# Kernel optimization log

Measured on AMD Instinct MI355X. Metric: run time of the kernel, lower is better.

## Reference

```python
import jax, jax.numpy as jnp
import numpy as np
import math

EMBED_DIM = 1024
NUM_HEADS = 16
HEAD_DIM = EMBED_DIM // NUM_HEADS
BATCH = 2
SEQ = 2048


def alibi_slopes(num_heads):
    def pow2_slopes(n):
        start = 2.0 ** (-(2.0 ** (-(math.log2(n) - 3))))
        return [start * (start ** i) for i in range(n)]
    if math.log2(num_heads).is_integer():
        s = pow2_slopes(num_heads)
    else:
        closest = 2 ** math.floor(math.log2(num_heads))
        s = pow2_slopes(closest)
        s += s[-1:] * (num_heads - closest)
    return jnp.asarray(s, dtype=jnp.float32)  # [H]


def setup_inputs() -> dict:
    key = jax.random.key(0)
    k1, k2, k3, k4, k5 = jax.random.split(key, 5)
    x = jax.random.normal(k1, (BATCH, SEQ, EMBED_DIM), dtype=jnp.float32)
    sd = 1.0 / math.sqrt(EMBED_DIM)
    Wqkv = jax.random.uniform(k2, (EMBED_DIM, 3 * EMBED_DIM), minval=-sd, maxval=sd, dtype=jnp.float32)
    bqkv = jax.random.uniform(k3, (3 * EMBED_DIM,), minval=-sd, maxval=sd, dtype=jnp.float32)
    Wout = jax.random.uniform(k4, (EMBED_DIM, EMBED_DIM), minval=-sd, maxval=sd, dtype=jnp.float32)
    bout = jax.random.uniform(k5, (EMBED_DIM,), minval=-sd, maxval=sd, dtype=jnp.float32)
    return {"x": x, "Wqkv": Wqkv, "bqkv": bqkv, "Wout": Wout, "bout": bout}


def reference(x, Wqkv, bqkv, Wout, bout):
    B, S, E = x.shape
    H, D = NUM_HEADS, HEAD_DIM
    qkv = x @ Wqkv + bqkv                       # [B,S,3E]
    qkv = qkv.reshape(B, S, H, 3 * D)
    q, k, v = jnp.split(qkv, 3, axis=-1)        # each [B,S,H,D]
    scores = jnp.einsum('bqhd,bkhd->bhqk', q, k) / math.sqrt(D)
    # ALiBi bias: distance[i,j] = j - i, scaled per-head
    pos = jnp.arange(S)
    distance = (pos[None, :] - pos[:, None]).astype(jnp.float32)  # [S,S]
    scores = scores + alibi_slopes(H)[None, :, None, None] * distance[None, None, :, :]
    attn = jax.nn.softmax(scores, axis=-1)      # [B,H,S,S]
    out = jnp.einsum('bhqk,bkhd->bqhd', attn, v).reshape(B, S, E)
    out = out @ Wout + bout
    return out, attn
```

## Files before the change

kernel.cpp:

```cpp
#include <hip/hip_runtime.h>

#define BATCH 2
#define SEQ   2048
#define EMB   1024
#define NH    16
#define HD    64

typedef __attribute__((ext_vector_type(8))) _Float16 half8;
typedef __attribute__((ext_vector_type(4))) _Float16 half4;
typedef __attribute__((ext_vector_type(4))) float floatx4;

#define LOG2E 1.44269504088896f

#if __has_builtin(__builtin_amdgcn_exp2f)
__device__ __forceinline__ float fexp2(float x) { return __builtin_amdgcn_exp2f(x); }
#else
__device__ __forceinline__ float fexp2(float x) { return exp2f(x); }
#endif

__global__ __launch_bounds__(256)
void cvt_f16(const float* __restrict__ in, _Float16* __restrict__ out, int n8) {
    int i = blockIdx.x * 256 + threadIdx.x;
    if (i >= n8) return;
    float4 a = ((const float4*)in)[2 * i];
    float4 b = ((const float4*)in)[2 * i + 1];
    half8 h = {(_Float16)a.x, (_Float16)a.y, (_Float16)a.z, (_Float16)a.w,
               (_Float16)b.x, (_Float16)b.y, (_Float16)b.z, (_Float16)b.w};
    ((half8*)out)[i] = h;
}

__global__ __launch_bounds__(256)
void transpose_f16(const float* __restrict__ W, _Float16* __restrict__ o,
                   int K, int N) {
    __shared__ float t[32][33];
    const int n0 = blockIdx.x * 32, k0 = blockIdx.y * 32;
    const int r = threadIdx.x >> 3, c4 = (threadIdx.x & 7) * 4;
    float4 v = *(const float4*)&W[(size_t)(k0 + r) * N + n0 + c4];
    t[r][c4 + 0] = v.x; t[r][c4 + 1] = v.y;
    t[r][c4 + 2] = v.z; t[r][c4 + 3] = v.w;
    __syncthreads();
    half4 hv;
#pragma unroll
    for (int j = 0; j < 4; ++j) hv[j] = (_Float16)t[c4 + j][r];
    *(half4*)&o[(size_t)(n0 + r) * K + k0 + c4] = hv;
}

#define ALD 40

__global__ __launch_bounds__(256)
void gemm_qkv_mfma(const _Float16* __restrict__ Xh, const _Float16* __restrict__ Wh,
                   const float* __restrict__ bias,
                   _Float16* __restrict__ Qh, _Float16* __restrict__ Kh,
                   _Float16* __restrict__ Vh) {
    const int K = EMB;
    __shared__ _Float16 Ah[2][128 * ALD];
    __shared__ _Float16 Bh[2][128 * ALD];

    const int tid  = threadIdx.x;
    const int wave = tid >> 6, lane = tid & 63;
    const int quad = lane >> 4, lp = lane & 15;

    const int linear = blockIdx.y * 24 + blockIdx.x;
    const int swz = (linear & 7) * 96 + (linear >> 3);
    const int bx = swz % 24, by = swz / 24;
    const int row0 = by * 128, col0 = bx * 128;
    const int wm = (wave >> 1) * 64, wn = (wave & 1) * 64;

    const int srow = tid >> 2, sseg = (tid & 3) * 8;

    floatx4 acc[4][4];
#pragma unroll
    for (int i = 0; i < 4; ++i)
#pragma unroll
        for (int j = 0; j < 4; ++j) acc[i][j] = (floatx4){0.f, 0.f, 0.f, 0.f};

    uint4 a0 = *(const uint4*)&Xh[(size_t)(row0 + srow) * K + sseg];
    uint4 a1 = *(const uint4*)&Xh[(size_t)(row0 + srow + 64) * K + sseg];
    uint4 b0 = *(const uint4*)&Wh[(size_t)(col0 + srow) * K + sseg];
    uint4 b1 = *(const uint4*)&Wh[(size_t)(col0 + srow + 64) * K + sseg];
    *(uint4*)&Ah[0][srow * ALD + sseg] = a0;
    *(uint4*)&Ah[0][(srow + 64) * ALD + sseg] = a1;
    *(uint4*)&Bh[0][srow * ALD + sseg] = b0;
    *(uint4*)&Bh[0][(srow + 64) * ALD + sseg] = b1;

    int cur = 0;
    for (int k0 = 0; k0 < K; k0 += 32) {
        __syncthreads();
        if (k0 + 32 < K) {
            a0 = *(const uint4*)&Xh[(size_t)(row0 + srow) * K + k0 + 32 + sseg];
            a1 = *(const uint4*)&Xh[(size_t)(row0 + srow + 64) * K + k0 + 32 + sseg];
            b0 = *(const uint4*)&Wh[(size_t)(col0 + srow) * K + k0 + 32 + sseg];
            b1 = *(const uint4*)&Wh[(size_t)(col0 + srow + 64) * K + k0 + 32 + sseg];
        }

        half8 ah[4];
#pragma unroll
        for (int mi = 0; mi < 4; ++mi)
            ah[mi] = *(const half8*)&Ah[cur][(wm + mi * 16 + lp) * ALD + quad * 8];
#pragma unroll
        for (int ni = 0; ni < 4; ++ni) {
            half8 bh = *(const half8*)&Bh[cur][(wn + ni * 16 + lp) * ALD + quad * 8];
#pragma unroll
            for (int mi = 0; mi < 4; ++mi)
                acc[mi][ni] = __builtin_amdgcn_mfma_f32_16x16x32_f16(
                    ah[mi], bh, acc[mi][ni], 0, 0, 0);
        }

        if (k0 + 32 < K) {
            *(uint4*)&Ah[cur ^ 1][srow * ALD + sseg] = a0;
            *(uint4*)&Ah[cur ^ 1][(srow + 64) * ALD + sseg] = a1;
            *(uint4*)&Bh[cur ^ 1][srow * ALD + sseg] = b0;
            *(uint4*)&Bh[cur ^ 1][(srow + 64) * ALD + sseg] = b1;
            cur ^= 1;
        }
    }

#pragma unroll
    for (int ni = 0; ni < 4; ++ni) {
        const int c = col0 + wn + ni * 16 + lp;
        const int h = c / 192;
        const int rem = c - h * 192;
        const int which = rem >> 6;
        const int d = rem & 63;
        _Float16* __restrict__ P = (which == 0) ? Qh : (which == 1) ? Kh : Vh;
        const float bb = bias[c];
#pragma unroll
        for (int mi = 0; mi < 4; ++mi) {
            floatx4 a = acc[mi][ni];
#pragma unroll
            for (int r = 0; r < 4; ++r) {
                int m = row0 + wm + mi * 16 + quad * 4 + r;
                int b = m >> 11, s = m & (SEQ - 1);
                P[((size_t)(b * NH + h) * SEQ + s) * HD + d] =
                    (_Float16)(a[r] + bb);
            }
        }
    }
}

__global__ __launch_bounds__(256)
void gemm_out_mfma(const _Float16* __restrict__ Ch, const _Float16* __restrict__ Oh,
                   const float* __restrict__ bias, float* __restrict__ out) {
    const int K = EMB, N = EMB;
    __shared__ _Float16 Ah[2][128 * ALD];
    __shared__ _Float16 Bh[2][128 * ALD];

    const int tid  = threadIdx.x;
    const int wave = tid >> 6, lane = tid & 63;
    const int quad = lane >> 4, lp = lane & 15;

    const int linear = blockIdx.y * 8 + blockIdx.x;
    const int swz = (linear & 7) * 32 + (linear >> 3);
    const int bx = swz & 7, by = swz >> 3;
    const int row0 = by * 128, col0 = bx * 128;
    const int wm = (wave >> 1) * 64, wn = (wave & 1) * 64;

    const int srow = tid >> 2, sseg = (tid & 3) * 8;

    floatx4 acc[4][4];
#pragma unroll
    for (int i = 0; i < 4; ++i)
#pragma unroll
        for (int j = 0; j < 4; ++j) acc[i][j] = (floatx4){0.f, 0.f, 0.f, 0.f};

    uint4 a0 = *(const uint4*)&Ch[(size_t)(row0 + srow) * K + sseg];
    uint4 a1 = *(const uint4*)&Ch[(size_t)(row0 + srow + 64) * K + sseg];
    uint4 b0 = *(const uint4*)&Oh[(size_t)(col0 + srow) * K + sseg];
    uint4 b1 = *(const uint4*)&Oh[(size_t)(col0 + srow + 64) * K + sseg];
    *(uint4*)&Ah[0][srow * ALD + sseg] = a0;
    *(uint4*)&Ah[0][(srow + 64) * ALD + sseg] = a1;
    *(uint4*)&Bh[0][srow * ALD + sseg] = b0;
    *(uint4*)&Bh[0][(srow + 64) * ALD + sseg] = b1;

    int cur = 0;
    for (int k0 = 0; k0 < K; k0 += 32) {
        __syncthreads();
        if (k0 + 32 < K) {
            a0 = *(const uint4*)&Ch[(size_t)(row0 + srow) * K + k0 + 32 + sseg];
            a1 = *(const uint4*)&Ch[(size_t)(row0 + srow + 64) * K + k0 + 32 + sseg];
            b0 = *(const uint4*)&Oh[(size_t)(col0 + srow) * K + k0 + 32 + sseg];
            b1 = *(const uint4*)&Oh[(size_t)(col0 + srow + 64) * K + k0 + 32 + sseg];
        }

        half8 ah[4];
#pragma unroll
        for (int mi = 0; mi < 4; ++mi)
            ah[mi] = *(const half8*)&Ah[cur][(wm + mi * 16 + lp) * ALD + quad * 8];
#pragma unroll
        for (int ni = 0; ni < 4; ++ni) {
            half8 bh = *(const half8*)&Bh[cur][(wn + ni * 16 + lp) * ALD + quad * 8];
#pragma unroll
            for (int mi = 0; mi < 4; ++mi)
                acc[mi][ni] = __builtin_amdgcn_mfma_f32_16x16x32_f16(
                    ah[mi], bh, acc[mi][ni], 0, 0, 0);
        }

        if (k0 + 32 < K) {
            *(uint4*)&Ah[cur ^ 1][srow * ALD + sseg] = a0;
            *(uint4*)&Ah[cur ^ 1][(srow + 64) * ALD + sseg] = a1;
            *(uint4*)&Bh[cur ^ 1][srow * ALD + sseg] = b0;
            *(uint4*)&Bh[cur ^ 1][(srow + 64) * ALD + sseg] = b1;
            cur ^= 1;
        }
    }

#pragma unroll
    for (int ni = 0; ni < 4; ++ni) {
        const int c = col0 + wn + ni * 16 + lp;
        const float bb = bias[c];
#pragma unroll
        for (int mi = 0; mi < 4; ++mi) {
            floatx4 a = acc[mi][ni];
#pragma unroll
            for (int r = 0; r < 4; ++r) {
                int m = row0 + wm + mi * 16 + quad * 4 + r;
                out[(size_t)m * N + c] = a[r] + bb;
            }
        }
    }
}

#define QT 128
#define KT 64
#define LDST 72
#define NTILE (SEQ / KT)

__global__ __launch_bounds__(512)
void attn_mfma(const _Float16* __restrict__ Qh,
               const _Float16* __restrict__ Kh,
               const _Float16* __restrict__ Vh,
               float* __restrict__ attn,
               _Float16* __restrict__ ctx) {
    __shared__ _Float16 ksb[2][KT * LDST];
    __shared__ _Float16 vtb[2][HD * LDST];
    __shared__ _Float16 ps[QT * LDST];

    const int tid  = threadIdx.x;
    const int wave = tid >> 6, lane = tid & 63;
    const int quad = lane >> 4, lp = lane & 15;
    const int q0 = blockIdx.x * QT;
    const int bh = blockIdx.y;
    const int h  = bh & (NH - 1);
    const float slope2 = exp2f(-0.5f * (float)(h + 1)) * LOG2E;
    const float scale2 = 0.125f * LOG2E;

    const _Float16* Qbase = Qh + ((size_t)bh * SEQ + q0) * HD;
    const _Float16* Kbase = Kh + (size_t)bh * SEQ * HD;
    const _Float16* Vbase = Vh + (size_t)bh * SEQ * HD;

    const half8 qa0 = *(const half8*)&Qbase[(size_t)(16 * wave + lp) * HD + quad * 8];
    const half8 qa1 = *(const half8*)&Qbase[(size_t)(16 * wave + lp) * HD + 32 + quad * 8];

    const int qg = q0 + 16 * wave + lp;
    const float aq = -slope2 * (float)qg;

    const int srow = tid >> 3, sseg = tid & 7;
    const int kvx = srow ^ (sseg << 3);

    float m0 = -1e30f, mxv = -1e30f, lsum = 0.f;

    uint4 kreg = *(const uint4*)&Kbase[(size_t)srow * HD + sseg * 8];
    *(uint4*)&ksb[0][srow * LDST + sseg * 8] = kreg;
    __syncthreads();

    int cur = 0;
    for (int kt = 0; kt < NTILE; ++kt) {
        if (kt) __syncthreads();
        if (kt + 1 < NTILE)
            kreg = *(const uint4*)&Kbase[(size_t)(kt + 1) * KT * HD +
                                         (size_t)srow * HD + sseg * 8];
        const _Float16* ks = ksb[cur];

        floatx4 cc[4];
        __builtin_amdgcn_s_setprio(1);
#pragma unroll
        for (int t = 0; t < 4; ++t) {
            half8 b0 = *(const half8*)&ks[(16 * t + lp) * LDST + quad * 8];
            half8 b1 = *(const half8*)&ks[(16 * t + lp) * LDST + 32 + quad * 8];
            floatx4 c = {0.f, 0.f, 0.f, 0.f};
            c = __builtin_amdgcn_mfma_f32_16x16x32_f16(b0, qa0, c, 0, 0, 0);
            cc[t] = __builtin_amdgcn_mfma_f32_16x16x32_f16(b1, qa1, c, 0, 0, 0);
        }
        __builtin_amdgcn_s_setprio(0);
#pragma unroll
        for (int t = 0; t < 4; ++t) {
            float kb = (float)(kt * KT + 16 * t + 4 * quad);
            float s0 = fmaf(cc[t][0], scale2, fmaf(slope2, kb,       aq));
            float s1 = fmaf(cc[t][1], scale2, fmaf(slope2, kb + 1.f, aq));
            float s2 = fmaf(cc[t][2], scale2, fmaf(slope2, kb + 2.f, aq));
            float s3 = fmaf(cc[t][3], scale2, fmaf(slope2, kb + 3.f, aq));
            float tm = fmaxf(fmaxf(s0, s1), fmaxf(s2, s3));
            mxv = fmaxf(mxv, tm);
            if (mxv > m0 + 8.f) {
                lsum *= fexp2(m0 - mxv);
                m0 = mxv;
            }
            lsum += fexp2(s0 - m0) + fexp2(s1 - m0) +
                    fexp2(s2 - m0) + fexp2(s3 - m0);
        }

        if (kt + 1 < NTILE) {
            *(uint4*)&ksb[cur ^ 1][srow * LDST + sseg * 8] = kreg;
            cur ^= 1;
        }
    }

    float off2;
    {
        float mm = mxv;
        float ll = lsum * fexp2(m0 - mm);
#pragma unroll
        for (int off = 16; off < 64; off <<= 1) {
            float mo = __shfl_xor(mm, off);
            float lo = __shfl_xor(ll, off);
            float mn = fmaxf(mm, mo);
            ll = ll * fexp2(mm - mn) + lo * fexp2(mo - mn);
            mm = mn;
        }
        off2 = mm + __log2f(ll);
    }

    floatx4 o[4];
#pragma unroll
    for (int t = 0; t < 4; ++t) o[t] = (floatx4){0.f, 0.f, 0.f, 0.f};

    float* arow = attn + (size_t)bh * SEQ * SEQ +
                  (size_t)(q0 + 16 * wave + lp) * SEQ + 4 * quad;
    const float aq2 = aq - off2;

    __syncthreads();
    uint4 vreg;
    kreg = *(const uint4*)&Kbase[(size_t)srow * HD + sseg * 8];
    vreg = *(const uint4*)&Vbase[(size_t)srow * HD + sseg * 8];
    *(uint4*)&ksb[0][srow * LDST + sseg * 8] = kreg;
    {
        union { uint4 u; _Float16 e[8]; } vv; vv.u = vreg;
#pragma unroll
        for (int j = 0; j < 8; ++j)
            vtb[0][(sseg * 8 + j) * LDST + kvx] = vv.e[j];
    }
    __syncthreads();

    cur = 0;
    for (int kt = 0; kt < NTILE; ++kt) {
        if (kt) __syncthreads();
        if (kt + 1 < NTILE) {
            size_t goff = (size_t)(kt + 1) * KT * HD + (size_t)srow * HD + sseg * 8;
            kreg = *(const uint4*)&Kbase[goff];
            vreg = *(const uint4*)&Vbase[goff];
        }
        const _Float16* ks = ksb[cur];
        const _Float16* vt = vtb[cur];

        __builtin_amdgcn_s_setprio(1);
#pragma unroll
        for (int t = 0; t < 4; ++t) {
            half8 b0 = *(const half8*)&ks[(16 * t + lp) * LDST + quad * 8];
            half8 b1 = *(const half8*)&ks[(16 * t + lp) * LDST + 32 + quad * 8];
            floatx4 c = {0.f, 0.f, 0.f, 0.f};
            c = __builtin_amdgcn_mfma_f32_16x16x32_f16(b0, qa0, c, 0, 0, 0);
            c = __builtin_amdgcn_mfma_f32_16x16x32_f16(b1, qa1, c, 0, 0, 0);
            float kb = (float)(kt * KT + 16 * t + 4 * quad);
            float p0 = fexp2(fmaf(c[0], scale2, fmaf(slope2, kb,       aq2)));
            float p1 = fexp2(fmaf(c[1], scale2, fmaf(slope2, kb + 1.f, aq2)));
            float p2 = fexp2(fmaf(c[2], scale2, fmaf(slope2, kb + 2.f, aq2)));
            float p3 = fexp2(fmaf(c[3], scale2, fmaf(slope2, kb + 3.f, aq2)));
            float4 pw = {p0, p1, p2, p3};
            *(float4*)&arow[kt * KT + 16 * t] = pw;
            const int col = 16 * t + 4 * quad;
            half4 ph = {(_Float16)p0, (_Float16)p1, (_Float16)p2, (_Float16)p3};
            *(half4*)&ps[(16 * wave + lp) * LDST + col] = ph;
        }
        __builtin_amdgcn_s_setprio(0);

        half8 pa0 = *(const half8*)&ps[(16 * wave + lp) * LDST + quad * 8];
        half8 pa1 = *(const half8*)&ps[(16 * wave + lp) * LDST + 32 + quad * 8];
        __builtin_amdgcn_s_setprio(1);
#pragma unroll
        for (int t = 0; t < 4; ++t) {
            int g = 2 * t + (lp >> 3);
            half8 vb0 = *(const half8*)&vt[(16 * t + lp) * LDST + ((quad ^ g) << 3)];
            half8 vb1 = *(const half8*)&vt[(16 * t + lp) * LDST + (((quad + 4) ^ g) << 3)];
            o[t] = __builtin_amdgcn_mfma_f32_16x16x32_f16(pa0, vb0, o[t], 0, 0, 0);
            o[t] = __builtin_amdgcn_mfma_f32_16x16x32_f16(pa1, vb1, o[t], 0, 0, 0);
        }
        __builtin_amdgcn_s_setprio(0);

        if (kt + 1 < NTILE) {
            *(uint4*)&ksb[cur ^ 1][srow * LDST + sseg * 8] = kreg;
            union { uint4 u; _Float16 e[8]; } vv; vv.u = vreg;
#pragma unroll
            for (int j = 0; j < 8; ++j)
                vtb[cur ^ 1][(sseg * 8 + j) * LDST + kvx] = vv.e[j];
            cur ^= 1;
        }
    }

    const int b = bh >> 4;
#pragma unroll
    for (int t = 0; t < 4; ++t)
#pragma unroll
        for (int r = 0; r < 4; ++r)
            ctx[((size_t)(b * SEQ + q0 + 16 * wave + quad * 4 + r)) * EMB +
                h * HD + 16 * t + lp] = (_Float16)o[t][r];
}


extern "C" void kernel_launch(void* const* d_in, const int* in_sizes, int n_in,
                              void* d_out, int out_size, void* d_ws, size_t ws_size,
                              hipStream_t stream) {
    const float* x    = (const float*)d_in[0];
    const float* Wqkv = (const float*)d_in[1];
    const float* bqkv = (const float*)d_in[2];
    const float* Wout = (const float*)d_in[3];
    const float* bout = (const float*)d_in[4];

    float* out  = (float*)d_out;
    float* attn = out + (size_t)BATCH * SEQ * EMB;

    const size_t HE = (size_t)BATCH * NH * SEQ * HD;
    const size_t XE = (size_t)BATCH * SEQ * EMB;
    _Float16* Qh = (_Float16*)d_ws;
    _Float16* Kh = Qh + HE;
    _Float16* Vh = Kh + HE;
    _Float16* Ch = Vh + HE;
    _Float16* Xh = Ch + XE;
    _Float16* Wh = Xh + XE;
    _Float16* Oh = Wh + (size_t)3 * EMB * EMB;

    cvt_f16<<<dim3(2048), dim3(256), 0, stream>>>(x, Xh, (int)(XE / 8));
    transpose_f16<<<dim3(96, 32), dim3(256), 0, stream>>>(Wqkv, Wh, EMB, 3 * EMB);
    transpose_f16<<<dim3(32, 32), dim3(256), 0, stream>>>(Wout, Oh, EMB, EMB);

    gemm_qkv_mfma<<<dim3(24, 32), dim3(256), 0, stream>>>(
        Xh, Wh, bqkv, Qh, Kh, Vh);

    attn_mfma<<<dim3(SEQ / QT, BATCH * NH), dim3(512), 0, stream>>>(
        Qh, Kh, Vh, attn, Ch);

    gemm_out_mfma<<<dim3(8, 32), dim3(256), 0, stream>>>(Ch, Oh, bout, out);
}
```

Measured before the change: 258.8 us.

## Load GEMM tiles directly to LDS and relax attention barriers

Both the QKV and output-projection GEMMs now use global_load_lds to move their double-buffered tiles straight from global memory into LDS, with no register staging. The LDS row stride drops from 40 to 32 halves so that each lane's 16-byte destination is contiguous with the lane index, which the direct load requires. The attention kernel replaces __syncthreads with a barrier that waits only on lgkmcnt, so in-flight global prefetches into registers are not drained at every tile. The trade-off is that the unpadded GEMM tiles may cause LDS bank conflicts on the fragment reads.

```diff
diff --git a/kernel.cpp b/kernel.cpp
--- a/kernel.cpp
+++ b/kernel.cpp
@@ -17,6 +17,19 @@
 #else
 __device__ __forceinline__ float fexp2(float x) { return exp2f(x); }
 #endif
+
+__device__ __forceinline__ void gl2lds16(const _Float16* gp, _Float16* lp_) {
+    __builtin_amdgcn_global_load_lds(
+        (const __attribute__((address_space(1))) unsigned int*)gp,
+        (__attribute__((address_space(3))) unsigned int*)lp_,
+        16, 0, 0);
+}
+
+__device__ __forceinline__ void lds_barrier() {
+    asm volatile("s_waitcnt lgkmcnt(0)" ::: "memory");
+    __builtin_amdgcn_s_barrier();
+    __builtin_amdgcn_sched_barrier(0);
+}
 
 __global__ __launch_bounds__(256)
 void cvt_f16(const float* __restrict__ in, _Float16* __restrict__ out, int n8) {
@@ -45,7 +58,7 @@
     *(half4*)&o[(size_t)(n0 + r) * K + k0 + c4] = hv;
 }
 
-#define ALD 40
+#define ALD 32
 
 __global__ __launch_bounds__(256)
 void gemm_qkv_mfma(const _Float16* __restrict__ Xh, const _Float16* __restrict__ Wh,
@@ -74,23 +87,24 @@
 #pragma unroll
         for (int j = 0; j < 4; ++j) acc[i][j] = (floatx4){0.f, 0.f, 0.f, 0.f};
 
-    uint4 a0 = *(const uint4*)&Xh[(size_t)(row0 + srow) * K + sseg];
-    uint4 a1 = *(const uint4*)&Xh[(size_t)(row0 + srow + 64) * K + sseg];
-    uint4 b0 = *(const uint4*)&Wh[(size_t)(col0 + srow) * K + sseg];
-    uint4 b1 = *(const uint4*)&Wh[(size_t)(col0 + srow + 64) * K + sseg];
-    *(uint4*)&Ah[0][srow * ALD + sseg] = a0;
-    *(uint4*)&Ah[0][(srow + 64) * ALD + sseg] = a1;
-    *(uint4*)&Bh[0][srow * ALD + sseg] = b0;
-    *(uint4*)&Bh[0][(srow + 64) * ALD + sseg] = b1;
+    gl2lds16(&Xh[(size_t)(row0 + srow) * K + sseg],      &Ah[0][srow * ALD + sseg]);
+    gl2lds16(&Xh[(size_t)(row0 + srow + 64) * K + sseg], &Ah[0][(srow + 64) * ALD + sseg]);
+    gl2lds16(&Wh[(size_t)(col0 + srow) * K + sseg],      &Bh[0][srow * ALD + sseg]);
+    gl2lds16(&Wh[(size_t)(col0 + srow + 64) * K + sseg], &Bh[0][(srow + 64) * ALD + sseg]);
 
     int cur = 0;
     for (int k0 = 0; k0 < K; k0 += 32) {
         __syncthreads();
         if (k0 + 32 < K) {
-            a0 = *(const uint4*)&Xh[(size_t)(row0 + srow) * K + k0 + 32 + sseg];
-            a1 = *(const uint4*)&Xh[(size_t)(row0 + srow + 64) * K + k0 + 32 + sseg];
-            b0 = *(const uint4*)&Wh[(size_t)(col0 + srow) * K + k0 + 32 + sseg];
-            b1 = *(const uint4*)&Wh[(size_t)(col0 + srow + 64) * K + k0 + 32 + sseg];
+            int kn = k0 + 32;
+            gl2lds16(&Xh[(size_t)(row0 + srow) * K + kn + sseg],
+                     &Ah[cur ^ 1][srow * ALD + sseg]);
+            gl2lds16(&Xh[(size_t)(row0 + srow + 64) * K + kn + sseg],
+                     &Ah[cur ^ 1][(srow + 64) * ALD + sseg]);
+            gl2lds16(&Wh[(size_t)(col0 + srow) * K + kn + sseg],
+                     &Bh[cur ^ 1][srow * ALD + sseg]);
+            gl2lds16(&Wh[(size_t)(col0 + srow + 64) * K + kn + sseg],
+                     &Bh[cur ^ 1][(srow + 64) * ALD + sseg]);
         }
 
         half8 ah[4];
@@ -106,13 +120,7 @@
                     ah[mi], bh, acc[mi][ni], 0, 0, 0);
         }
 
-        if (k0 + 32 < K) {
-            *(uint4*)&Ah[cur ^ 1][srow * ALD + sseg] = a0;
-            *(uint4*)&Ah[cur ^ 1][(srow + 64) * ALD + sseg] = a1;
-            *(uint4*)&Bh[cur ^ 1][srow * ALD + sseg] = b0;
-            *(uint4*)&Bh[cur ^ 1][(srow + 64) * ALD + sseg] = b1;
-            cur ^= 1;
-        }
+        if (k0 + 32 < K) cur ^= 1;
     }
 
 #pragma unroll
@@ -163,23 +171,24 @@
 #pragma unroll
         for (int j = 0; j < 4; ++j) acc[i][j] = (floatx4){0.f, 0.f, 0.f, 0.f};
 
-    uint4 a0 = *(const uint4*)&Ch[(size_t)(row0 + srow) * K + sseg];
-    uint4 a1 = *(const uint4*)&Ch[(size_t)(row0 + srow + 64) * K + sseg];
-    uint4 b0 = *(const uint4*)&Oh[(size_t)(col0 + srow) * K + sseg];
-    uint4 b1 = *(const uint4*)&Oh[(size_t)(col0 + srow + 64) * K + sseg];
-    *(uint4*)&Ah[0][srow * ALD + sseg] = a0;
-    *(uint4*)&Ah[0][(srow + 64) * ALD + sseg] = a1;
-    *(uint4*)&Bh[0][srow * ALD + sseg] = b0;
-    *(uint4*)&Bh[0][(srow + 64) * ALD + sseg] = b1;
+    gl2lds16(&Ch[(size_t)(row0 + srow) * K + sseg],      &Ah[0][srow * ALD + sseg]);
+    gl2lds16(&Ch[(size_t)(row0 + srow + 64) * K + sseg], &Ah[0][(srow + 64) * ALD + sseg]);
+    gl2lds16(&Oh[(size_t)(col0 + srow) * K + sseg],      &Bh[0][srow * ALD + sseg]);
+    gl2lds16(&Oh[(size_t)(col0 + srow + 64) * K + sseg], &Bh[0][(srow + 64) * ALD + sseg]);
 
     int cur = 0;
     for (int k0 = 0; k0 < K; k0 += 32) {
         __syncthreads();
         if (k0 + 32 < K) {
-            a0 = *(const uint4*)&Ch[(size_t)(row0 + srow) * K + k0 + 32 + sseg];
-            a1 = *(const uint4*)&Ch[(size_t)(row0 + srow + 64) * K + k0 + 32 + sseg];
-            b0 = *(const uint4*)&Oh[(size_t)(col0 + srow) * K + k0 + 32 + sseg];
-            b1 = *(const uint4*)&Oh[(size_t)(col0 + srow + 64) * K + k0 + 32 + sseg];
+            int kn = k0 + 32;
+            gl2lds16(&Ch[(size_t)(row0 + srow) * K + kn + sseg],
+                     &Ah[cur ^ 1][srow * ALD + sseg]);
+            gl2lds16(&Ch[(size_t)(row0 + srow + 64) * K + kn + sseg],
+                     &Ah[cur ^ 1][(srow + 64) * ALD + sseg]);
+            gl2lds16(&Oh[(size_t)(col0 + srow) * K + kn + sseg],
+                     &Bh[cur ^ 1][srow * ALD + sseg]);
+            gl2lds16(&Oh[(size_t)(col0 + srow + 64) * K + kn + sseg],
+                     &Bh[cur ^ 1][(srow + 64) * ALD + sseg]);
         }
 
         half8 ah[4];
@@ -195,13 +204,7 @@
                     ah[mi], bh, acc[mi][ni], 0, 0, 0);
         }
 
-        if (k0 + 32 < K) {
-            *(uint4*)&Ah[cur ^ 1][srow * ALD + sseg] = a0;
-            *(uint4*)&Ah[cur ^ 1][(srow + 64) * ALD + sseg] = a1;
-            *(uint4*)&Bh[cur ^ 1][srow * ALD + sseg] = b0;
-            *(uint4*)&Bh[cur ^ 1][(srow + 64) * ALD + sseg] = b1;
-            cur ^= 1;
-        }
+        if (k0 + 32 < K) cur ^= 1;
     }
 
 #pragma unroll
@@ -261,11 +264,11 @@
 
     uint4 kreg = *(const uint4*)&Kbase[(size_t)srow * HD + sseg * 8];
     *(uint4*)&ksb[0][srow * LDST + sseg * 8] = kreg;
-    __syncthreads();
+    lds_barrier();
 
     int cur = 0;
     for (int kt = 0; kt < NTILE; ++kt) {
-        if (kt) __syncthreads();
+        if (kt) lds_barrier();
         if (kt + 1 < NTILE)
             kreg = *(const uint4*)&Kbase[(size_t)(kt + 1) * KT * HD +
                                          (size_t)srow * HD + sseg * 8];
@@ -328,7 +331,7 @@
                   (size_t)(q0 + 16 * wave + lp) * SEQ + 4 * quad;
     const float aq2 = aq - off2;
 
-    __syncthreads();
+    lds_barrier();
     uint4 vreg;
     kreg = *(const uint4*)&Kbase[(size_t)srow * HD + sseg * 8];
     vreg = *(const uint4*)&Vbase[(size_t)srow * HD + sseg * 8];
@@ -339,11 +342,11 @@
         for (int j = 0; j < 8; ++j)
             vtb[0][(sseg * 8 + j) * LDST + kvx] = vv.e[j];
     }
-    __syncthreads();
+    lds_barrier();
 
     cur = 0;
     for (int kt = 0; kt < NTILE; ++kt) {
-        if (kt) __syncthreads();
+        if (kt) lds_barrier();
         if (kt + 1 < NTILE) {
             size_t goff = (size_t)(kt + 1) * KT * HD + (size_t)srow * HD + sseg * 8;
             kreg = *(const uint4*)&Kbase[goff];
```

New measurement: 263.5 us. No clear change (+1.8%).

## Fuse x fp16 conversion into QKV GEMM, merge weight transposes, lighten barriers

Applied to the files above, without the earlier changes.

Removes the standalone x-to-fp16 conversion kernel: the QKV GEMM now loads fp32 x tiles directly and converts them to half before writing to LDS. The two weight transpose launches are combined into one kernel with a larger grid. The attention kernel's __syncthreads calls are replaced by a custom barrier that waits only on LDS counters, so outstanding global prefetches are not forced to drain. The aim is fewer launches and less intermediate traffic, at the cost of the GEMM reading twice as many bytes for x on each re-read.

```diff
diff --git a/kernel.cpp b/kernel.cpp
--- a/kernel.cpp
+++ b/kernel.cpp
@@ -18,22 +18,21 @@
 __device__ __forceinline__ float fexp2(float x) { return exp2f(x); }
 #endif
 
+__device__ __forceinline__ void lds_barrier() {
+    asm volatile("s_waitcnt lgkmcnt(0)" ::: "memory");
+    __builtin_amdgcn_s_barrier();
+    __builtin_amdgcn_sched_barrier(0);
+}
+
 __global__ __launch_bounds__(256)
-void cvt_f16(const float* __restrict__ in, _Float16* __restrict__ out, int n8) {
-    int i = blockIdx.x * 256 + threadIdx.x;
-    if (i >= n8) return;
-    float4 a = ((const float4*)in)[2 * i];
-    float4 b = ((const float4*)in)[2 * i + 1];
-    half8 h = {(_Float16)a.x, (_Float16)a.y, (_Float16)a.z, (_Float16)a.w,
-               (_Float16)b.x, (_Float16)b.y, (_Float16)b.z, (_Float16)b.w};
-    ((half8*)out)[i] = h;
-}
-
-__global__ __launch_bounds__(256)
-void transpose_f16(const float* __restrict__ W, _Float16* __restrict__ o,
-                   int K, int N) {
+void transpose_both(const float* __restrict__ Wqkv, const float* __restrict__ Wout,
+                    _Float16* __restrict__ Wh, _Float16* __restrict__ Oh) {
     __shared__ float t[32][33];
-    const int n0 = blockIdx.x * 32, k0 = blockIdx.y * 32;
+    const int K = EMB;
+    const float* W; _Float16* o; int N, n0;
+    if (blockIdx.x < 96) { W = Wqkv; o = Wh; N = 3 * EMB; n0 = blockIdx.x * 32; }
+    else                 { W = Wout; o = Oh; N = EMB;     n0 = (blockIdx.x - 96) * 32; }
+    const int k0 = blockIdx.y * 32;
     const int r = threadIdx.x >> 3, c4 = (threadIdx.x & 7) * 4;
     float4 v = *(const float4*)&W[(size_t)(k0 + r) * N + n0 + c4];
     t[r][c4 + 0] = v.x; t[r][c4 + 1] = v.y;
@@ -47,8 +46,14 @@
 
 #define ALD 40
 
+__device__ __forceinline__ half8 cvt8(float4 lo, float4 hi) {
+    half8 h = {(_Float16)lo.x, (_Float16)lo.y, (_Float16)lo.z, (_Float16)lo.w,
+               (_Float16)hi.x, (_Float16)hi.y, (_Float16)hi.z, (_Float16)hi.w};
+    return h;
+}
+
 __global__ __launch_bounds__(256)
-void gemm_qkv_mfma(const _Float16* __restrict__ Xh, const _Float16* __restrict__ Wh,
+void gemm_qkv_mfma(const float* __restrict__ X, const _Float16* __restrict__ Wh,
                    const float* __restrict__ bias,
                    _Float16* __restrict__ Qh, _Float16* __restrict__ Kh,
                    _Float16* __restrict__ Vh) {
@@ -74,12 +79,14 @@
 #pragma unroll
         for (int j = 0; j < 4; ++j) acc[i][j] = (floatx4){0.f, 0.f, 0.f, 0.f};
 
-    uint4 a0 = *(const uint4*)&Xh[(size_t)(row0 + srow) * K + sseg];
-    uint4 a1 = *(const uint4*)&Xh[(size_t)(row0 + srow + 64) * K + sseg];
+    float4 a0l = *(const float4*)&X[(size_t)(row0 + srow) * K + sseg];
+    float4 a0h = *(const float4*)&X[(size_t)(row0 + srow) * K + sseg + 4];
+    float4 a1l = *(const float4*)&X[(size_t)(row0 + srow + 64) * K + sseg];
+    float4 a1h = *(const float4*)&X[(size_t)(row0 + srow + 64) * K + sseg + 4];
     uint4 b0 = *(const uint4*)&Wh[(size_t)(col0 + srow) * K + sseg];
     uint4 b1 = *(const uint4*)&Wh[(size_t)(col0 + srow + 64) * K + sseg];
-    *(uint4*)&Ah[0][srow * ALD + sseg] = a0;
-    *(uint4*)&Ah[0][(srow + 64) * ALD + sseg] = a1;
+    *(half8*)&Ah[0][srow * ALD + sseg] = cvt8(a0l, a0h);
+    *(half8*)&Ah[0][(srow + 64) * ALD + sseg] = cvt8(a1l, a1h);
     *(uint4*)&Bh[0][srow * ALD + sseg] = b0;
     *(uint4*)&Bh[0][(srow + 64) * ALD + sseg] = b1;
 
@@ -87,10 +94,13 @@
     for (int k0 = 0; k0 < K; k0 += 32) {
         __syncthreads();
         if (k0 + 32 < K) {
-            a0 = *(const uint4*)&Xh[(size_t)(row0 + srow) * K + k0 + 32 + sseg];
-            a1 = *(const uint4*)&Xh[(size_t)(row0 + srow + 64) * K + k0 + 32 + sseg];
-            b0 = *(const uint4*)&Wh[(size_t)(col0 + srow) * K + k0 + 32 + sseg];
-            b1 = *(const uint4*)&Wh[(size_t)(col0 + srow + 64) * K + k0 + 32 + sseg];
+            int kn = k0 + 32;
+            a0l = *(const float4*)&X[(size_t)(row0 + srow) * K + kn + sseg];
+            a0h = *(const float4*)&X[(size_t)(row0 + srow) * K + kn + sseg + 4];
+            a1l = *(const float4*)&X[(size_t)(row0 + srow + 64) * K + kn + sseg];
+            a1h = *(const float4*)&X[(size_t)(row0 + srow + 64) * K + kn + sseg + 4];
+            b0 = *(const uint4*)&Wh[(size_t)(col0 + srow) * K + kn + sseg];
+            b1 = *(const uint4*)&Wh[(size_t)(col0 + srow + 64) * K + kn + sseg];
         }
 
         half8 ah[4];
@@ -107,8 +117,8 @@
         }
 
         if (k0 + 32 < K) {
-            *(uint4*)&Ah[cur ^ 1][srow * ALD + sseg] = a0;
-            *(uint4*)&Ah[cur ^ 1][(srow + 64) * ALD + sseg] = a1;
+            *(half8*)&Ah[cur ^ 1][srow * ALD + sseg] = cvt8(a0l, a0h);
+            *(half8*)&Ah[cur ^ 1][(srow + 64) * ALD + sseg] = cvt8(a1l, a1h);
             *(uint4*)&Bh[cur ^ 1][srow * ALD + sseg] = b0;
             *(uint4*)&Bh[cur ^ 1][(srow + 64) * ALD + sseg] = b1;
             cur ^= 1;
@@ -261,11 +271,11 @@
 
     uint4 kreg = *(const uint4*)&Kbase[(size_t)srow * HD + sseg * 8];
     *(uint4*)&ksb[0][srow * LDST + sseg * 8] = kreg;
-    __syncthreads();
+    lds_barrier();
 
     int cur = 0;
     for (int kt = 0; kt < NTILE; ++kt) {
-        if (kt) __syncthreads();
+        if (kt) lds_barrier();
         if (kt + 1 < NTILE)
             kreg = *(const uint4*)&Kbase[(size_t)(kt + 1) * KT * HD +
                                          (size_t)srow * HD + sseg * 8];
@@ -328,7 +338,7 @@
                   (size_t)(q0 + 16 * wave + lp) * SEQ + 4 * quad;
     const float aq2 = aq - off2;
 
-    __syncthreads();
+    lds_barrier();
     uint4 vreg;
     kreg = *(const uint4*)&Kbase[(size_t)srow * HD + sseg * 8];
     vreg = *(const uint4*)&Vbase[(size_t)srow * HD + sseg * 8];
@@ -339,11 +349,11 @@
         for (int j = 0; j < 8; ++j)
             vtb[0][(sseg * 8 + j) * LDST + kvx] = vv.e[j];
     }
-    __syncthreads();
+    lds_barrier();
 
     cur = 0;
     for (int kt = 0; kt < NTILE; ++kt) {
-        if (kt) __syncthreads();
+        if (kt) lds_barrier();
         if (kt + 1 < NTILE) {
             size_t goff = (size_t)(kt + 1) * KT * HD + (size_t)srow * HD + sseg * 8;
             kreg = *(const uint4*)&Kbase[goff];
@@ -424,16 +434,13 @@
     _Float16* Kh = Qh + HE;
     _Float16* Vh = Kh + HE;
     _Float16* Ch = Vh + HE;
-    _Float16* Xh = Ch + XE;
-    _Float16* Wh = Xh + XE;
+    _Float16* Wh = Ch + XE;
     _Float16* Oh = Wh + (size_t)3 * EMB * EMB;
 
-    cvt_f16<<<dim3(2048), dim3(256), 0, stream>>>(x, Xh, (int)(XE / 8));
-    transpose_f16<<<dim3(96, 32), dim3(256), 0, stream>>>(Wqkv, Wh, EMB, 3 * EMB);
-    transpose_f16<<<dim3(32, 32), dim3(256), 0, stream>>>(Wout, Oh, EMB, EMB);
+    transpose_both<<<dim3(128, 32), dim3(256), 0, stream>>>(Wqkv, Wout, Wh, Oh);
 
     gemm_qkv_mfma<<<dim3(24, 32), dim3(256), 0, stream>>>(
-        Xh, Wh, bqkv, Qh, Kh, Vh);
+        x, Wh, bqkv, Qh, Kh, Vh);
 
     attn_mfma<<<dim3(SEQ / QT, BATCH * NH), dim3(512), 0, stream>>>(
         Qh, Kh, Vh, attn, Ch);
```

Measured after the change: 288.6 us. +11.5%, slower.
